# Kernel optimization log

Measured on AMD Instinct MI355X. Metric: run time of the kernel, lower is better.

The kernel has to match this reference:

```python
import jax, jax.numpy as jnp
import numpy as np

RADIUS = 0.2
NSAMPLE = 32


def setup_inputs() -> dict:
    key = jax.random.key(0)
    k1, k2 = jax.random.split(key)
    B, N = 8, 4096
    xyz = jax.random.uniform(k1, (B, N, 3), dtype=jnp.float32)
    xyz_new = jax.random.uniform(k2, (B, N, 3), dtype=jnp.float32)  # ignored by forward, kept for signature fidelity
    return {"xyz": xyz, "xyz_new": xyz_new}


def _ball_query(radius, nsample, xyz, new_xyz):
    # xyz: [B, N, 3] source points; new_xyz: [B, M, 3] query centers.
    # Returns idx: [B, M, nsample] int32, matching pointnet2 CUDA ball_query:
    # first `nsample` indices j (in increasing j order) with ||q - p_j||^2 < r^2;
    # unused slots are filled with the first valid index.
    B, N, _ = xyz.shape
    sq_src = jnp.sum(xyz * xyz, axis=-1)          # [B, N]
    sq_q = jnp.sum(new_xyz * new_xyz, axis=-1)    # [B, M]
    # d2[b, m, n] = ||q_m - p_n||^2
    d2 = sq_q[:, :, None] + sq_src[:, None, :] - 2.0 * jnp.einsum(
        "bmc,bnc->bmn", new_xyz, xyz)             # [B, M, N]
    mask = d2 < (radius * radius)                 # [B, M, N] bool
    # key = index j when within radius, else sentinel N (sorts to the end)
    idx_range = jnp.arange(N, dtype=jnp.int32)
    keys = jnp.where(mask, idx_range[None, None, :], jnp.int32(N))
    sorted_keys = jnp.sort(keys, axis=-1)[..., :nsample]  # [B, M, nsample]
    first = sorted_keys[..., 0:1]                 # first valid index (pad value)
    idx = jnp.where(sorted_keys < N, sorted_keys, first)
    return idx.astype(jnp.int32)


def reference(xyz, xyz_new):
    # Faithful to the module: ball_query(radius, nsample, xyz, xyz) — xyz_new unused.
    return _ball_query(RADIUS, NSAMPLE, xyz, xyz)
```

## Files before the change

### kernel.cpp

```cpp
#include <hip/hip_runtime.h>
#include <cstdint>


#define BQ_N    4096
#define BQ_B    8
#define BQ_NS   32
#define BQ_R2   0.04f

__device__ __forceinline__ float sq_plain(float x, float y, float z) {
    float r, t;
    asm("v_mul_f32 %0, %2, %2\n\t"
        "v_mul_f32 %1, %3, %3\n\t"
        "v_add_f32 %0, %0, %1\n\t"
        "v_mul_f32 %1, %4, %4\n\t"
        "v_add_f32 %0, %0, %1"
        : "=&v"(r), "=&v"(t)
        : "v"(x), "v"(y), "v"(z));
    return r;
}

__device__ __forceinline__ float d2_mixed(float qx, float qy, float qz, float sqq,
                                          float sx, float sy, float sz, float sqs) {
    float r, t;
    asm("v_mul_f32 %0, %2, %5\n\t"
        "v_fma_f32 %0, %3, %6, %0\n\t"
        "v_fma_f32 %0, %4, %7, %0\n\t"
        "v_add_f32 %0, %0, %0\n\t"
        "v_add_f32 %1, %8, %9\n\t"
        "v_sub_f32 %0, %1, %0"
        : "=&v"(r), "=&v"(t)
        : "v"(qx), "v"(qy), "v"(qz), "v"(sx), "v"(sy), "v"(sz),
          "v"(sqq), "v"(sqs));
    return r;
}

__device__ __forceinline__ void scan1g(const float* __restrict__ src, int lane,
                                       const float4& q, int c,
                                       uint64_t& word, int& wpre, int& found) {
    float X[4], Y[4], Z[4];
    #pragma unroll
    for (int u = 0; u < 4; ++u) {
        const int k = (c << 2) + u;
        const float* ptr = src + (size_t)(((k << 6) + lane) * 3);
        X[u] = ptr[0]; Y[u] = ptr[1]; Z[u] = ptr[2];
    }
    #pragma unroll
    for (int u = 0; u < 4; ++u) {
        const int k = (c << 2) + u;
        const float sqs = sq_plain(X[u], Y[u], Z[u]);
        const float d2  = d2_mixed(q.x, q.y, q.z, q.w, X[u], Y[u], Z[u], sqs);
        const uint64_t bal = __ballot(d2 < BQ_R2);
        if (lane == k) { word = bal; wpre = found; }
        found += (int)__popcll(bal);
    }
}

__device__ __forceinline__ void scan2g(const float* __restrict__ src, int lane,
                                       const float4& q0, const float4& q1,
                                       int c0, int c1,
                                       uint64_t& w0, uint64_t& w1,
                                       int& p0, int& p1, int& f0, int& f1) {
    int c = c0;
    while (c < c1) {
        float X[4], Y[4], Z[4];
        #pragma unroll
        for (int u = 0; u < 4; ++u) {
            const int k = (c << 2) + u;
            const float* ptr = src + (size_t)(((k << 6) + lane) * 3);
            X[u] = ptr[0]; Y[u] = ptr[1]; Z[u] = ptr[2];
        }
        #pragma unroll
        for (int u = 0; u < 4; ++u) {
            const int k = (c << 2) + u;
            const float sqs = sq_plain(X[u], Y[u], Z[u]);
            const float d20 = d2_mixed(q0.x, q0.y, q0.z, q0.w,
                                       X[u], Y[u], Z[u], sqs);
            const float d21 = d2_mixed(q1.x, q1.y, q1.z, q1.w,
                                       X[u], Y[u], Z[u], sqs);
            const uint64_t b0 = __ballot(d20 < BQ_R2);
            const uint64_t b1 = __ballot(d21 < BQ_R2);
            if (lane == k) { w0 = b0; w1 = b1; p0 = f0; p1 = f1; }
            f0 += (int)__popcll(b0);
            f1 += (int)__popcll(b1);
        }
        ++c;
        if (f0 >= BQ_NS || f1 >= BQ_NS) break;
    }
    for (int ca = c; ca < c1 && f0 < BQ_NS; ++ca) scan1g(src, lane, q0, ca, w0, p0, f0);
    for (int cb = c; cb < c1 && f1 < BQ_NS; ++cb) scan1g(src, lane, q1, cb, w1, p1, f1);
}

__device__ __forceinline__ void emit_query(int* __restrict__ orow, int lane,
                                           uint64_t word, int wpre, int total) {
    uint64_t w = word;
    int pos = wpre;
    while (w != 0ull && pos < BQ_NS) {
        const int bit = __builtin_ctzll(w);
        orow[pos] = (lane << 6) + bit;
        w &= (w - 1);
        ++pos;
    }
    if (total < BQ_NS) {
        int first;
        const uint64_t nz = __ballot(word != 0ull);
        if (nz == 0ull) {
            first = BQ_N;
        } else {
            const int fl = __builtin_ctzll(nz);
            const uint64_t fw = __shfl(word, fl);
            first = (fl << 6) + __builtin_ctzll(fw);
        }
        if (lane >= total && lane < BQ_NS) orow[lane] = first;
    }
}

__global__ __launch_bounds__(128, 4)
void ball_query_kernel(const float* __restrict__ xyz, int* __restrict__ out)
{
    const int b     = blockIdx.x >> 9;
    const int qbase = (blockIdx.x & 511) << 3;
    const int lane  = threadIdx.x & 63;
    const int wid   = threadIdx.x >> 6;
    const float* __restrict__ src = xyz + (size_t)b * BQ_N * 3;
    int* __restrict__ outb = out + (size_t)(b * BQ_N) * BQ_NS;

    float4 Q[4];
    #pragma unroll
    for (int j = 0; j < 4; ++j) {
        const int m = qbase + (wid << 2) + j;
        const float x = src[3 * m + 0];
        const float y = src[3 * m + 1];
        const float z = src[3 * m + 2];
        Q[j] = make_float4(x, y, z, sq_plain(x, y, z));
    }

    uint64_t W[4] = {0, 0, 0, 0};
    int      P[4] = {0, 0, 0, 0};
    int      F[4] = {0, 0, 0, 0};

    scan2g(src, lane, Q[0], Q[1], 0, 16, W[0], W[1], P[0], P[1], F[0], F[1]);
    scan2g(src, lane, Q[2], Q[3], 0, 16, W[2], W[3], P[2], P[3], F[2], F[3]);

    #pragma unroll
    for (int j = 0; j < 4; ++j) {
        const int m = qbase + (wid << 2) + j;
        emit_query(outb + (size_t)m * BQ_NS, lane, W[j], P[j], F[j]);
    }
}

extern "C" void kernel_launch(void* const* d_in, const int* in_sizes, int n_in,
                              void* d_out, int out_size, void* d_ws, size_t ws_size,
                              hipStream_t stream)
{
    const float* xyz = (const float*)d_in[0];
    int* out = (int*)d_out;
    hipLaunchKernelGGL(ball_query_kernel, dim3(4096), dim3(128), 0, stream,
                       xyz, out);
}
```

Baseline: 79.09 us.

## Pack points into float4 with precomputed norms and double-buffer chunk loads

Adds a pre-pass kernel that converts the xyz array into float4 records holding x, y, z and the squared norm, written to workspace. The main kernel then loads one 16-byte vector per point instead of three strided scalars and skips recomputing the norm for each query. The scan loop is also software-pipelined, prefetching the next chunk while the current one is processed. This costs an extra kernel launch and workspace traffic, and falls back to the old kernel when no workspace is provided.

```diff
diff --git a/kernel.cpp b/kernel.cpp
--- a/kernel.cpp
+++ b/kernel.cpp
@@ -6,6 +6,7 @@
 #define BQ_B    8
 #define BQ_NS   32
 #define BQ_R2   0.04f
+#define BQ_NC   16
 
 __device__ __forceinline__ float sq_plain(float x, float y, float z) {
     float r, t;
@@ -34,9 +35,146 @@
     return r;
 }
 
+
+__global__ __launch_bounds__(256)
+void pack_kernel(const float* __restrict__ xyz, float4* __restrict__ pk)
+{
+    const int i = blockIdx.x * 256 + threadIdx.x;
+    const float x = xyz[3 * i + 0];
+    const float y = xyz[3 * i + 1];
+    const float z = xyz[3 * i + 2];
+    pk[i] = make_float4(x, y, z, sq_plain(x, y, z));
+}
+
+__device__ __forceinline__ void load_chunk(const float4* __restrict__ pp,
+                                           int lane, int c, float4 S[4])
+{
+    #pragma unroll
+    for (int u = 0; u < 4; ++u)
+        S[u] = pp[(((c << 2) + u) << 6) + lane];
+}
+
+__device__ __forceinline__ void proc2(const float4 S[4], int lane, int c,
+                                      const float4& q0, const float4& q1,
+                                      uint64_t& w0, uint64_t& w1,
+                                      int& p0, int& p1, int& f0, int& f1)
+{
+    #pragma unroll
+    for (int u = 0; u < 4; ++u) {
+        const int k = (c << 2) + u;
+        const float d20 = d2_mixed(q0.x, q0.y, q0.z, q0.w,
+                                   S[u].x, S[u].y, S[u].z, S[u].w);
+        const float d21 = d2_mixed(q1.x, q1.y, q1.z, q1.w,
+                                   S[u].x, S[u].y, S[u].z, S[u].w);
+        const uint64_t b0 = __ballot(d20 < BQ_R2);
+        const uint64_t b1 = __ballot(d21 < BQ_R2);
+        if (lane == k) { w0 = b0; w1 = b1; p0 = f0; p1 = f1; }
+        f0 += (int)__popcll(b0);
+        f1 += (int)__popcll(b1);
+    }
+}
+
+__device__ __forceinline__ void scan1p(const float4* __restrict__ pp, int lane,
+                                       const float4& q, int c,
+                                       uint64_t& word, int& wpre, int& found)
+{
+    float4 S[4];
+    load_chunk(pp, lane, c, S);
+    #pragma unroll
+    for (int u = 0; u < 4; ++u) {
+        const int k = (c << 2) + u;
+        const float d2 = d2_mixed(q.x, q.y, q.z, q.w,
+                                  S[u].x, S[u].y, S[u].z, S[u].w);
+        const uint64_t bal = __ballot(d2 < BQ_R2);
+        if (lane == k) { word = bal; wpre = found; }
+        found += (int)__popcll(bal);
+    }
+}
+
+__device__ __forceinline__ void scan2p(const float4* __restrict__ pp, int lane,
+                                       const float4& q0, const float4& q1,
+                                       uint64_t& w0, uint64_t& w1,
+                                       int& p0, int& p1, int& f0, int& f1)
+{
+    float4 A[4], B[4];
+    load_chunk(pp, lane, 0, A);
+    int c = 0;
+    for (;;) {
+        int cn = (c + 1 < BQ_NC) ? c + 1 : c;
+        load_chunk(pp, lane, cn, B);
+        proc2(A, lane, c, q0, q1, w0, w1, p0, p1, f0, f1);
+        ++c;
+        if (c >= BQ_NC || f0 >= BQ_NS || f1 >= BQ_NS) break;
+
+        cn = (c + 1 < BQ_NC) ? c + 1 : c;
+        load_chunk(pp, lane, cn, A);
+        proc2(B, lane, c, q0, q1, w0, w1, p0, p1, f0, f1);
+        ++c;
+        if (c >= BQ_NC || f0 >= BQ_NS || f1 >= BQ_NS) break;
+    }
+    for (int ca = c; ca < BQ_NC && f0 < BQ_NS; ++ca) scan1p(pp, lane, q0, ca, w0, p0, f0);
+    for (int cb = c; cb < BQ_NC && f1 < BQ_NS; ++cb) scan1p(pp, lane, q1, cb, w1, p1, f1);
+}
+
+__device__ __forceinline__ void emit_query(int* __restrict__ orow, int lane,
+                                           uint64_t word, int wpre, int total)
+{
+    uint64_t w = word;
+    int pos = wpre;
+    while (w != 0ull && pos < BQ_NS) {
+        const int bit = __builtin_ctzll(w);
+        orow[pos] = (lane << 6) + bit;
+        w &= (w - 1);
+        ++pos;
+    }
+    if (total < BQ_NS) {
+        int first;
+        const uint64_t nz = __ballot(word != 0ull);
+        if (nz == 0ull) {
+            first = BQ_N;
+        } else {
+            const int fl = __builtin_ctzll(nz);
+            const uint64_t fw = __shfl(word, fl);
+            first = (fl << 6) + __builtin_ctzll(fw);
+        }
+        if (lane >= total && lane < BQ_NS) orow[lane] = first;
+    }
+}
+
+__global__ __launch_bounds__(128, 4)
+void ball_query_packed(const float4* __restrict__ pk, int* __restrict__ out)
+{
+    const int b     = blockIdx.x >> 9;
+    const int qbase = (blockIdx.x & 511) << 3;
+    const int lane  = threadIdx.x & 63;
+    const int wid   = threadIdx.x >> 6;
+    const float4* __restrict__ pp = pk + (size_t)b * BQ_N;
+    int* __restrict__ outb = out + (size_t)(b * BQ_N) * BQ_NS;
+
+    float4 Q[4];
+    #pragma unroll
+    for (int j = 0; j < 4; ++j)
+        Q[j] = pp[qbase + (wid << 2) + j];
+
+    uint64_t W[4] = {0, 0, 0, 0};
+    int      P[4] = {0, 0, 0, 0};
+    int      F[4] = {0, 0, 0, 0};
+
+    scan2p(pp, lane, Q[0], Q[1], W[0], W[1], P[0], P[1], F[0], F[1]);
+    scan2p(pp, lane, Q[2], Q[3], W[2], W[3], P[2], P[3], F[2], F[3]);
+
+    #pragma unroll
+    for (int j = 0; j < 4; ++j) {
+        const int m = qbase + (wid << 2) + j;
+        emit_query(outb + (size_t)m * BQ_NS, lane, W[j], P[j], F[j]);
+    }
+}
+
+
 __device__ __forceinline__ void scan1g(const float* __restrict__ src, int lane,
                                        const float4& q, int c,
-                                       uint64_t& word, int& wpre, int& found) {
+                                       uint64_t& word, int& wpre, int& found)
+{
     float X[4], Y[4], Z[4];
     #pragma unroll
     for (int u = 0; u < 4; ++u) {
@@ -57,11 +195,11 @@
 
 __device__ __forceinline__ void scan2g(const float* __restrict__ src, int lane,
                                        const float4& q0, const float4& q1,
-                                       int c0, int c1,
                                        uint64_t& w0, uint64_t& w1,
-                                       int& p0, int& p1, int& f0, int& f1) {
-    int c = c0;
-    while (c < c1) {
+                                       int& p0, int& p1, int& f0, int& f1)
+{
+    int c = 0;
+    while (c < BQ_NC) {
         float X[4], Y[4], Z[4];
         #pragma unroll
         for (int u = 0; u < 4; ++u) {
@@ -73,10 +211,8 @@
         for (int u = 0; u < 4; ++u) {
             const int k = (c << 2) + u;
             const float sqs = sq_plain(X[u], Y[u], Z[u]);
-            const float d20 = d2_mixed(q0.x, q0.y, q0.z, q0.w,
-                                       X[u], Y[u], Z[u], sqs);
-            const float d21 = d2_mixed(q1.x, q1.y, q1.z, q1.w,
-                                       X[u], Y[u], Z[u], sqs);
+            const float d20 = d2_mixed(q0.x, q0.y, q0.z, q0.w, X[u], Y[u], Z[u], sqs);
+            const float d21 = d2_mixed(q1.x, q1.y, q1.z, q1.w, X[u], Y[u], Z[u], sqs);
             const uint64_t b0 = __ballot(d20 < BQ_R2);
             const uint64_t b1 = __ballot(d21 < BQ_R2);
             if (lane == k) { w0 = b0; w1 = b1; p0 = f0; p1 = f1; }
@@ -86,32 +222,8 @@
         ++c;
         if (f0 >= BQ_NS || f1 >= BQ_NS) break;
     }
-    for (int ca = c; ca < c1 && f0 < BQ_NS; ++ca) scan1g(src, lane, q0, ca, w0, p0, f0);
-    for (int cb = c; cb < c1 && f1 < BQ_NS; ++cb) scan1g(src, lane, q1, cb, w1, p1, f1);
-}
-
-__device__ __forceinline__ void emit_query(int* __restrict__ orow, int lane,
-                                           uint64_t word, int wpre, int total) {
-    uint64_t w = word;
-    int pos = wpre;
-    while (w != 0ull && pos < BQ_NS) {
-        const int bit = __builtin_ctzll(w);
-        orow[pos] = (lane << 6) + bit;
-        w &= (w - 1);
-        ++pos;
-    }
-    if (total < BQ_NS) {
-        int first;
-        const uint64_t nz = __ballot(word != 0ull);
-        if (nz == 0ull) {
-            first = BQ_N;
-        } else {
-            const int fl = __builtin_ctzll(nz);
-            const uint64_t fw = __shfl(word, fl);
-            first = (fl << 6) + __builtin_ctzll(fw);
-        }
-        if (lane >= total && lane < BQ_NS) orow[lane] = first;
-    }
+    for (int ca = c; ca < BQ_NC && f0 < BQ_NS; ++ca) scan1g(src, lane, q0, ca, w0, p0, f0);
+    for (int cb = c; cb < BQ_NC && f1 < BQ_NS; ++cb) scan1g(src, lane, q1, cb, w1, p1, f1);
 }
 
 __global__ __launch_bounds__(128, 4)
@@ -138,8 +250,8 @@
     int      P[4] = {0, 0, 0, 0};
     int      F[4] = {0, 0, 0, 0};
 
-    scan2g(src, lane, Q[0], Q[1], 0, 16, W[0], W[1], P[0], P[1], F[0], F[1]);
-    scan2g(src, lane, Q[2], Q[3], 0, 16, W[2], W[3], P[2], P[3], F[2], F[3]);
+    scan2g(src, lane, Q[0], Q[1], W[0], W[1], P[0], P[1], F[0], F[1]);
+    scan2g(src, lane, Q[2], Q[3], W[2], W[3], P[2], P[3], F[2], F[3]);
 
     #pragma unroll
     for (int j = 0; j < 4; ++j) {
@@ -148,12 +260,22 @@
     }
 }
 
+
 extern "C" void kernel_launch(void* const* d_in, const int* in_sizes, int n_in,
                               void* d_out, int out_size, void* d_ws, size_t ws_size,
                               hipStream_t stream)
 {
     const float* xyz = (const float*)d_in[0];
     int* out = (int*)d_out;
-    hipLaunchKernelGGL(ball_query_kernel, dim3(4096), dim3(128), 0, stream,
-                       xyz, out);
-}
+    const size_t pk_bytes = (size_t)BQ_B * BQ_N * sizeof(float4);
+    if (d_ws != nullptr && ws_size >= pk_bytes) {
+        float4* pk = (float4*)d_ws;
+        hipLaunchKernelGGL(pack_kernel, dim3((BQ_B * BQ_N) / 256), dim3(256),
+                           0, stream, xyz, pk);
+        hipLaunchKernelGGL(ball_query_packed, dim3(4096), dim3(128), 0, stream,
+                           pk, out);
+    } else {
+        hipLaunchKernelGGL(ball_query_kernel, dim3(4096), dim3(128), 0, stream,
+                           xyz, out);
+    }
+}
```

New measurement: 81.04 us. +2.5%, slower.

## Process eight queries per wave with double-buffered chunk loads and per-query early skip

Applied to the files above, without the earlier changes.

Each wave now handles eight query points instead of four, so every source-point chunk it loads serves more distance tests. Chunk loads are double-buffered so the next chunk is fetched while the current one is processed. Each query skips work once it has 32 neighbours, checked with a wave-uniform readfirstlane, and the loop exits when all eight are done. The grid is halved to match. The costs are higher register pressure from 8 queries plus two buffers, fewer waves in flight, and a wave that keeps scanning until its slowest query finishes.

```diff
diff --git a/kernel.cpp b/kernel.cpp
--- a/kernel.cpp
+++ b/kernel.cpp
@@ -6,6 +6,7 @@
 #define BQ_B    8
 #define BQ_NS   32
 #define BQ_R2   0.04f
+#define BQ_NC   16
 
 __device__ __forceinline__ float sq_plain(float x, float y, float z) {
     float r, t;
@@ -34,64 +35,56 @@
     return r;
 }
 
-__device__ __forceinline__ void scan1g(const float* __restrict__ src, int lane,
-                                       const float4& q, int c,
-                                       uint64_t& word, int& wpre, int& found) {
-    float X[4], Y[4], Z[4];
+__device__ __forceinline__ int rfl(int v) {
+    return __builtin_amdgcn_readfirstlane(v);
+}
+
+__device__ __forceinline__ void loadc(const float* __restrict__ src, int lane,
+                                      int c, float X[4], float Y[4], float Z[4])
+{
     #pragma unroll
     for (int u = 0; u < 4; ++u) {
         const int k = (c << 2) + u;
-        const float* ptr = src + (size_t)(((k << 6) + lane) * 3);
-        X[u] = ptr[0]; Y[u] = ptr[1]; Z[u] = ptr[2];
-    }
-    #pragma unroll
-    for (int u = 0; u < 4; ++u) {
-        const int k = (c << 2) + u;
-        const float sqs = sq_plain(X[u], Y[u], Z[u]);
-        const float d2  = d2_mixed(q.x, q.y, q.z, q.w, X[u], Y[u], Z[u], sqs);
-        const uint64_t bal = __ballot(d2 < BQ_R2);
-        if (lane == k) { word = bal; wpre = found; }
-        found += (int)__popcll(bal);
+        const float* p = src + (size_t)(((k << 6) + lane) * 3);
+        X[u] = p[0]; Y[u] = p[1]; Z[u] = p[2];
     }
 }
 
-__device__ __forceinline__ void scan2g(const float* __restrict__ src, int lane,
-                                       const float4& q0, const float4& q1,
-                                       int c0, int c1,
-                                       uint64_t& w0, uint64_t& w1,
-                                       int& p0, int& p1, int& f0, int& f1) {
-    int c = c0;
-    while (c < c1) {
-        float X[4], Y[4], Z[4];
-        #pragma unroll
-        for (int u = 0; u < 4; ++u) {
-            const int k = (c << 2) + u;
-            const float* ptr = src + (size_t)(((k << 6) + lane) * 3);
-            X[u] = ptr[0]; Y[u] = ptr[1]; Z[u] = ptr[2];
+__device__ __forceinline__ void procc(const float X[4], const float Y[4],
+                                      const float Z[4], int lane, int c,
+                                      const float4 Q[8], uint64_t W[8],
+                                      int P[8], int F[8])
+{
+    float SQ[4];
+    #pragma unroll
+    for (int u = 0; u < 4; ++u) SQ[u] = sq_plain(X[u], Y[u], Z[u]);
+
+    #pragma unroll
+    for (int j = 0; j < 8; ++j) {
+        if (rfl(F[j]) < BQ_NS) {
+            #pragma unroll
+            for (int u = 0; u < 4; ++u) {
+                const int k = (c << 2) + u;
+                const float d2 = d2_mixed(Q[j].x, Q[j].y, Q[j].z, Q[j].w,
+                                          X[u], Y[u], Z[u], SQ[u]);
+                const uint64_t bal = __ballot(d2 < BQ_R2);
+                if (lane == k) { W[j] = bal; P[j] = F[j]; }
+                F[j] += (int)__popcll(bal);
+            }
         }
-        #pragma unroll
-        for (int u = 0; u < 4; ++u) {
-            const int k = (c << 2) + u;
-            const float sqs = sq_plain(X[u], Y[u], Z[u]);
-            const float d20 = d2_mixed(q0.x, q0.y, q0.z, q0.w,
-                                       X[u], Y[u], Z[u], sqs);
-            const float d21 = d2_mixed(q1.x, q1.y, q1.z, q1.w,
-                                       X[u], Y[u], Z[u], sqs);
-            const uint64_t b0 = __ballot(d20 < BQ_R2);
-            const uint64_t b1 = __ballot(d21 < BQ_R2);
-            if (lane == k) { w0 = b0; w1 = b1; p0 = f0; p1 = f1; }
-            f0 += (int)__popcll(b0);
-            f1 += (int)__popcll(b1);
-        }
-        ++c;
-        if (f0 >= BQ_NS || f1 >= BQ_NS) break;
     }
-    for (int ca = c; ca < c1 && f0 < BQ_NS; ++ca) scan1g(src, lane, q0, ca, w0, p0, f0);
-    for (int cb = c; cb < c1 && f1 < BQ_NS; ++cb) scan1g(src, lane, q1, cb, w1, p1, f1);
+}
+
+__device__ __forceinline__ bool alldone(const int F[8]) {
+    int m = F[0];
+    #pragma unroll
+    for (int j = 1; j < 8; ++j) m = min(m, F[j]);
+    return rfl(m) >= BQ_NS;
 }
 
 __device__ __forceinline__ void emit_query(int* __restrict__ orow, int lane,
-                                           uint64_t word, int wpre, int total) {
+                                           uint64_t word, int wpre, int total)
+{
     uint64_t w = word;
     int pos = wpre;
     while (w != 0ull && pos < BQ_NS) {
@@ -117,35 +110,47 @@
 __global__ __launch_bounds__(128, 4)
 void ball_query_kernel(const float* __restrict__ xyz, int* __restrict__ out)
 {
-    const int b     = blockIdx.x >> 9;
-    const int qbase = (blockIdx.x & 511) << 3;
-    const int lane  = threadIdx.x & 63;
-    const int wid   = threadIdx.x >> 6;
+    const int b    = blockIdx.x >> 8;
+    const int wq   = ((blockIdx.x & 255) << 4) + ((threadIdx.x >> 6) << 3);
+    const int lane = threadIdx.x & 63;
     const float* __restrict__ src = xyz + (size_t)b * BQ_N * 3;
     int* __restrict__ outb = out + (size_t)(b * BQ_N) * BQ_NS;
 
-    float4 Q[4];
+    float4 Q[8];
     #pragma unroll
-    for (int j = 0; j < 4; ++j) {
-        const int m = qbase + (wid << 2) + j;
+    for (int j = 0; j < 8; ++j) {
+        const int m = wq + j;
         const float x = src[3 * m + 0];
         const float y = src[3 * m + 1];
         const float z = src[3 * m + 2];
         Q[j] = make_float4(x, y, z, sq_plain(x, y, z));
     }
 
-    uint64_t W[4] = {0, 0, 0, 0};
-    int      P[4] = {0, 0, 0, 0};
-    int      F[4] = {0, 0, 0, 0};
+    uint64_t W[8] = {0, 0, 0, 0, 0, 0, 0, 0};
+    int      P[8] = {0, 0, 0, 0, 0, 0, 0, 0};
+    int      F[8] = {0, 0, 0, 0, 0, 0, 0, 0};
 
-    scan2g(src, lane, Q[0], Q[1], 0, 16, W[0], W[1], P[0], P[1], F[0], F[1]);
-    scan2g(src, lane, Q[2], Q[3], 0, 16, W[2], W[3], P[2], P[3], F[2], F[3]);
+    float XA[4], YA[4], ZA[4], XB[4], YB[4], ZB[4];
+    loadc(src, lane, 0, XA, YA, ZA);
+
+    int c = 0;
+    for (;;) {
+        int cn = (c + 1 < BQ_NC) ? c + 1 : c;
+        loadc(src, lane, cn, XB, YB, ZB);
+        procc(XA, YA, ZA, lane, c, Q, W, P, F);
+        ++c;
+        if (c >= BQ_NC || alldone(F)) break;
+
+        cn = (c + 1 < BQ_NC) ? c + 1 : c;
+        loadc(src, lane, cn, XA, YA, ZA);
+        procc(XB, YB, ZB, lane, c, Q, W, P, F);
+        ++c;
+        if (c >= BQ_NC || alldone(F)) break;
+    }
 
     #pragma unroll
-    for (int j = 0; j < 4; ++j) {
-        const int m = qbase + (wid << 2) + j;
-        emit_query(outb + (size_t)m * BQ_NS, lane, W[j], P[j], F[j]);
-    }
+    for (int j = 0; j < 8; ++j)
+        emit_query(outb + (size_t)(wq + j) * BQ_NS, lane, W[j], P[j], F[j]);
 }
 
 extern "C" void kernel_launch(void* const* d_in, const int* in_sizes, int n_in,
@@ -154,6 +159,6 @@
 {
     const float* xyz = (const float*)d_in[0];
     int* out = (int*)d_out;
-    hipLaunchKernelGGL(ball_query_kernel, dim3(4096), dim3(128), 0, stream,
+    hipLaunchKernelGGL(ball_query_kernel, dim3(2048), dim3(128), 0, stream,
                        xyz, out);
 }
```

Measured after the change: 79.67 us. No clear change (+0.7%).
